# Performance work log

Measured on AMD Instinct MI355X. Metric: run time of the kernel, lower is better.

The kernel has to match this reference:

```python
import jax, jax.numpy as jnp
import numpy as np

NUM_GROUPS = 32
EPS = 1e-5


def group_norm(x, weight, bias):
    # x: (B, C, H, W, D); normalize per (group, spatial) per sample
    b, c, h, w, d = x.shape
    g = NUM_GROUPS
    xg = x.reshape(b, g, c // g, h, w, d)
    mean = xg.mean(axis=(2, 3, 4, 5), keepdims=True)
    var = xg.var(axis=(2, 3, 4, 5), keepdims=True)
    xg = (xg - mean) * jax.lax.rsqrt(var + EPS)
    xn = xg.reshape(b, c, h, w, d)
    return xn * weight[None, :, None, None, None] + bias[None, :, None, None, None]


def setup_inputs() -> dict:
    key = jax.random.key(0)
    ks = jax.random.split(key, 7)
    B, C, H, W, D = 4, 128, 16, 16, 16
    x = jax.random.normal(ks[0], (B, C, H, W, D), dtype=jnp.float32)
    gn_w = jnp.ones((C,), dtype=jnp.float32)
    gn_b = jnp.zeros((C,), dtype=jnp.float32)
    s = 1.0 / np.sqrt(C)
    qkv_w = jax.random.uniform(ks[1], (3 * C, C), minval=-s, maxval=s, dtype=jnp.float32)
    qkv_b = jax.random.uniform(ks[2], (3 * C,), minval=-s, maxval=s, dtype=jnp.float32)
    out_w = jax.random.uniform(ks[3], (C, C), minval=-s, maxval=s, dtype=jnp.float32)
    out_b = jax.random.uniform(ks[4], (C,), minval=-s, maxval=s, dtype=jnp.float32)
    return {"x": x, "gn_w": gn_w, "gn_b": gn_b, "qkv_w": qkv_w,
            "qkv_b": qkv_b, "out_w": out_w, "out_b": out_b}


def reference(x, gn_w, gn_b, qkv_w, qkv_b, out_w, out_b):
    b, c, h, w, d = x.shape
    n = h * w * d
    xn = group_norm(x, gn_w, gn_b)
    # 1x1x1 conv == pointwise linear over channels
    qkv = jnp.einsum('bchwd,oc->bohwd', xn, qkv_w) + qkv_b[None, :, None, None, None]
    q, k, v = jnp.split(qkv, 3, axis=1)
    q = q.transpose(0, 2, 3, 4, 1).reshape(b, n, c)   # (b, n, c)
    k = k.reshape(b, c, n)                             # (b, c, n)
    v = v.transpose(0, 2, 3, 4, 1).reshape(b, n, c)   # (b, n, c)
    scores = jnp.einsum('bnc,bcm->bnm', q, k) * (c ** -0.5)
    attn = jax.nn.softmax(scores, axis=-1)
    out = jnp.einsum('bnm,bmc->bnc', attn, v)          # (b, n, c)
    out = out.reshape(b, h, w, d, c).transpose(0, 4, 1, 2, 3)
    out = jnp.einsum('bchwd,oc->bohwd', out, out_w) + out_b[None, :, None, None, None]
    return out + x
```

## Files before the change

kernel.cpp:

```cpp
#include <hip/hip_runtime.h>

typedef unsigned short u16;
typedef __attribute__((ext_vector_type(8))) short bf16x8;
typedef __attribute__((ext_vector_type(4))) float f32x4;

__device__ __forceinline__ u16 f2bf(float f) {
    union { float f; unsigned u; } v; v.f = f;
    unsigned r = v.u + 0x7fffu + ((v.u >> 16) & 1u);
    return (u16)(r >> 16);
}

__device__ __forceinline__ void gload16(const u16* g, char* l) {
    __builtin_amdgcn_global_load_lds(
        (const __attribute__((address_space(1))) unsigned int*)g,
        (__attribute__((address_space(3))) unsigned int*)l, 16, 0, 0);
}

__global__ __launch_bounds__(256)
void k_stats(const float* __restrict__ x, float* __restrict__ mean, float* __restrict__ rstd)
{
    int bg = blockIdx.x, t = threadIdx.x;
    const float4* xp = (const float4*)(x + (size_t)bg * 16384);
    float s1 = 0.f, s2 = 0.f;
#pragma unroll
    for (int i = 0; i < 16; ++i) {
        float4 v = xp[i * 256 + t];
        s1 += v.x + v.y + v.z + v.w;
        s2 += v.x * v.x + v.y * v.y + v.z * v.z + v.w * v.w;
    }
#pragma unroll
    for (int off = 32; off >= 1; off >>= 1) {
        s1 += __shfl_xor(s1, off);
        s2 += __shfl_xor(s2, off);
    }
    __shared__ float a1[4], a2[4];
    if ((t & 63) == 0) { a1[t >> 6] = s1; a2[t >> 6] = s2; }
    __syncthreads();
    if (t == 0) {
        float t1 = a1[0] + a1[1] + a1[2] + a1[3];
        float t2 = a2[0] + a2[1] + a2[2] + a2[3];
        float mu = t1 * (1.f / 16384.f);
        float var = t2 * (1.f / 16384.f) - mu * mu;
        mean[bg] = mu;
        rstd[bg] = rsqrtf(var + 1e-5f);
    }
}

__global__ __launch_bounds__(384)
void k_qkv(const float* __restrict__ x, const float* __restrict__ gn_w, const float* __restrict__ gn_b,
           const float* __restrict__ qkv_w, const float* __restrict__ qkv_b,
           const float* __restrict__ mean, const float* __restrict__ rstd,
           u16* __restrict__ Qo, u16* __restrict__ Ko, u16* __restrict__ Vo)
{
    __shared__ float xn[128][64];
    int t = threadIdx.x;
    int b = blockIdx.x >> 6;
    int n0 = (blockIdx.x & 63) << 6;

    for (int e = t; e < 8192; e += 384) {
        int c = e >> 6, nn = e & 63;
        int bg = (b << 5) + (c >> 2);
        float sc = rstd[bg] * gn_w[c];
        float sh = gn_b[c] - mean[bg] * sc;
        xn[c][nn] = x[(size_t)(b * 128 + c) * 4096 + n0 + nn] * sc + sh;
    }
    __syncthreads();

    const int og = t >> 2;
    const int ng = t & 3;

    float acc[4][16];
#pragma unroll
    for (int i = 0; i < 4; ++i) {
        float bs = qkv_b[og * 4 + i];
#pragma unroll
        for (int j = 0; j < 16; ++j) acc[i][j] = bs;
    }

    const float4* wr0 = (const float4*)(qkv_w + (size_t)(og * 4 + 0) * 128);
    const float4* wr1 = (const float4*)(qkv_w + (size_t)(og * 4 + 1) * 128);
    const float4* wr2 = (const float4*)(qkv_w + (size_t)(og * 4 + 2) * 128);
    const float4* wr3 = (const float4*)(qkv_w + (size_t)(og * 4 + 3) * 128);

    for (int c4 = 0; c4 < 32; ++c4) {
        float4 w0 = wr0[c4], w1 = wr1[c4], w2 = wr2[c4], w3 = wr3[c4];
#pragma unroll
        for (int cc = 0; cc < 4; ++cc) {
            int c = c4 * 4 + cc;
            float v0 = (cc == 0) ? w0.x : (cc == 1) ? w0.y : (cc == 2) ? w0.z : w0.w;
            float v1 = (cc == 0) ? w1.x : (cc == 1) ? w1.y : (cc == 2) ? w1.z : w1.w;
            float v2 = (cc == 0) ? w2.x : (cc == 1) ? w2.y : (cc == 2) ? w2.z : w2.w;
            float v3 = (cc == 0) ? w3.x : (cc == 1) ? w3.y : (cc == 2) ? w3.z : w3.w;
#pragma unroll
            for (int j4 = 0; j4 < 4; ++j4) {
                float4 xv = *(const float4*)&xn[c][ng * 16 + j4 * 4];
#pragma unroll
                for (int jj = 0; jj < 4; ++jj) {
                    float xs = (jj == 0) ? xv.x : (jj == 1) ? xv.y : (jj == 2) ? xv.z : xv.w;
                    acc[0][j4 * 4 + jj] = fmaf(xs, v0, acc[0][j4 * 4 + jj]);
                    acc[1][j4 * 4 + jj] = fmaf(xs, v1, acc[1][j4 * 4 + jj]);
                    acc[2][j4 * 4 + jj] = fmaf(xs, v2, acc[2][j4 * 4 + jj]);
                    acc[3][j4 * 4 + jj] = fmaf(xs, v3, acc[3][j4 * 4 + jj]);
                }
            }
        }
    }

    const float qscale = 0.08838834764831845f * 1.4426950408889634f;
    if (og < 32) {
        size_t base = (size_t)(b * 4096 + n0 + ng * 16) * 128 + og * 4;
#pragma unroll
        for (int n = 0; n < 16; ++n) {
            uint2 pk;
            pk.x = ((unsigned)f2bf(acc[1][n] * qscale) << 16) | f2bf(acc[0][n] * qscale);
            pk.y = ((unsigned)f2bf(acc[3][n] * qscale) << 16) | f2bf(acc[2][n] * qscale);
            *(uint2*)&Qo[base + (size_t)n * 128] = pk;
        }
    } else if (og < 64) {
        size_t base = (size_t)(b * 4096 + n0 + ng * 16) * 128 + (og - 32) * 4;
#pragma unroll
        for (int n = 0; n < 16; ++n) {
            uint2 pk;
            pk.x = ((unsigned)f2bf(acc[1][n]) << 16) | f2bf(acc[0][n]);
            pk.y = ((unsigned)f2bf(acc[3][n]) << 16) | f2bf(acc[2][n]);
            *(uint2*)&Ko[base + (size_t)n * 128] = pk;
        }
    } else {
#pragma unroll
        for (int i = 0; i < 4; ++i) {
            size_t base = (size_t)(b * 128 + (og - 64) * 4 + i) * 4096 + n0 + ng * 16;
            uint4 pa, pb;
            pa.x = ((unsigned)f2bf(acc[i][1]) << 16) | f2bf(acc[i][0]);
            pa.y = ((unsigned)f2bf(acc[i][3]) << 16) | f2bf(acc[i][2]);
            pa.z = ((unsigned)f2bf(acc[i][5]) << 16) | f2bf(acc[i][4]);
            pa.w = ((unsigned)f2bf(acc[i][7]) << 16) | f2bf(acc[i][6]);
            pb.x = ((unsigned)f2bf(acc[i][9]) << 16) | f2bf(acc[i][8]);
            pb.y = ((unsigned)f2bf(acc[i][11]) << 16) | f2bf(acc[i][10]);
            pb.z = ((unsigned)f2bf(acc[i][13]) << 16) | f2bf(acc[i][12]);
            pb.w = ((unsigned)f2bf(acc[i][15]) << 16) | f2bf(acc[i][14]);
            *(uint4*)&Vo[base] = pa;
            *(uint4*)&Vo[base + 8] = pb;
        }
    }
}

__global__ __launch_bounds__(256, 2)
void k_attn(const u16* __restrict__ Qg, const u16* __restrict__ Kg, const u16* __restrict__ Vg,
            float* __restrict__ Opart, float* __restrict__ ml,
            int split, int kvlen, int iters)
{
    __shared__ __align__(16) u16 Kl[2][64 * 128];
    __shared__ __align__(16) u16 Vl[2][128 * 64];
    __shared__ __align__(16) u16 Pl[4 * 32 * 64];

    const int t = threadIdx.x;
    const int blk = blockIdx.x;
    const int half = blk % split;
    const int qt = (blk / split) & 31;
    const int b = blk / (split * 32);
    const int w = t >> 6;
    const int lane = t & 63;
    const int l15 = lane & 15;
    const int l4 = lane >> 4;
    const int q0 = qt << 7;
    const int swz = (l15 & 7) << 4;

    bf16x8 qf[2][4];
#pragma unroll
    for (int qh = 0; qh < 2; ++qh) {
        const u16* qb = Qg + (size_t)(b * 4096 + q0 + w * 32 + qh * 16 + l15) * 128 + l4 * 8;
#pragma unroll
        for (int kc = 0; kc < 4; ++kc) qf[qh][kc] = *(const bf16x8*)(qb + kc * 32);
    }
    f32x4 oac[2][8];
#pragma unroll
    for (int qh = 0; qh < 2; ++qh)
#pragma unroll
        for (int cf = 0; cf < 8; ++cf) oac[qh][cf] = (f32x4){0.f, 0.f, 0.f, 0.f};
    float m[2] = {-__builtin_inff(), -__builtin_inff()};
    float lsum[2] = {0.f, 0.f};

    const int kv0 = half * kvlen;
    char* plw = (char*)Pl + w * 4096;

    const int krow = lane >> 4;
    const int vrow = lane >> 3;
    const int kcolA = ((lane & 15) ^ krow) * 8;
    const int kcolB = ((lane & 15) ^ (krow + 4)) * 8;
    const int vcol  = ((lane & 7) ^ (vrow & 7)) * 8;
    const u16* KgB = Kg + (size_t)b * 4096 * 128;
    const u16* VgB = Vg + (size_t)b * 128 * 4096;

    auto STAGE = [&](int buf, int kvb) {
        char* kd = (char*)&Kl[buf][0] + w * 4096;
        char* vd = (char*)&Vl[buf][0] + w * 4096;
        const u16* kga = KgB + (size_t)(kvb + 16 * w) * 128;
        const u16* vga = VgB + kvb + (size_t)(32 * w) * 4096;
#pragma unroll
        for (int i = 0; i < 4; ++i) {
            gload16(kga + (size_t)(4 * i + krow) * 128 + ((i & 1) ? kcolB : kcolA),
                    kd + i * 1024);
            gload16(vga + (size_t)(8 * i + vrow) * 4096 + vcol,
                    vd + i * 1024);
        }
    };

    STAGE(0, kv0);
    __syncthreads();

    int cur = 0;
    for (int it = 0; it < iters; ++it) {
        if (it + 1 < iters) STAGE(cur ^ 1, kv0 + (it + 1) * 64);

        const char* kb = (const char*)&Kl[cur][0];
        f32x4 st[2][4];
        __builtin_amdgcn_s_setprio(1);
#pragma unroll
        for (int mt = 0; mt < 4; ++mt) {
            f32x4 s0 = (f32x4){0.f, 0.f, 0.f, 0.f};
            f32x4 s1 = (f32x4){0.f, 0.f, 0.f, 0.f};
#pragma unroll
            for (int kc = 0; kc < 4; ++kc) {
                bf16x8 kf = *(const bf16x8*)(kb + (mt * 16 + l15) * 256 +
                                             ((kc * 64 + l4 * 16) ^ swz));
                s0 = __builtin_amdgcn_mfma_f32_16x16x32_bf16(kf, qf[0][kc], s0, 0, 0, 0);
                s1 = __builtin_amdgcn_mfma_f32_16x16x32_bf16(kf, qf[1][kc], s1, 0, 0, 0);
            }
            st[0][mt] = s0;
            st[1][mt] = s1;
        }
        __builtin_amdgcn_s_setprio(0);

#pragma unroll
        for (int qh = 0; qh < 2; ++qh) {
            float pmax = -__builtin_inff();
#pragma unroll
            for (int mt = 0; mt < 4; ++mt)
                pmax = fmaxf(pmax, fmaxf(fmaxf(st[qh][mt][0], st[qh][mt][1]),
                                         fmaxf(st[qh][mt][2], st[qh][mt][3])));
            pmax = fmaxf(pmax, __shfl_xor(pmax, 16));
            pmax = fmaxf(pmax, __shfl_xor(pmax, 32));

            if (!__all(pmax - m[qh] <= 8.f)) {
                float nm = fmaxf(m[qh], pmax);
                float fr = __builtin_amdgcn_exp2f(m[qh] - nm);
                m[qh] = nm;
                lsum[qh] *= fr;
#pragma unroll
                for (int cf = 0; cf < 8; ++cf)
#pragma unroll
                    for (int r = 0; r < 4; ++r) oac[qh][cf][r] *= fr;
            }

            float rsum = 0.f;
            uint2 pw[4];
#pragma unroll
            for (int mt = 0; mt < 4; ++mt) {
                float p0 = __builtin_amdgcn_exp2f(st[qh][mt][0] - m[qh]);
                float p1 = __builtin_amdgcn_exp2f(st[qh][mt][1] - m[qh]);
                float p2 = __builtin_amdgcn_exp2f(st[qh][mt][2] - m[qh]);
                float p3 = __builtin_amdgcn_exp2f(st[qh][mt][3] - m[qh]);
                rsum += (p0 + p1) + (p2 + p3);
                pw[mt].x = ((unsigned)f2bf(p1) << 16) | f2bf(p0);
                pw[mt].y = ((unsigned)f2bf(p3) << 16) | f2bf(p2);
            }
            rsum += __shfl_xor(rsum, 16);
            rsum += __shfl_xor(rsum, 32);
            lsum[qh] += rsum;

#pragma unroll
            for (int mt = 0; mt < 4; ++mt)
                *(uint2*)(plw + (qh * 16 + l15) * 128 + ((mt * 32 + l4 * 8) ^ swz)) = pw[mt];
        }
        asm volatile("s_waitcnt lgkmcnt(0)" ::: "memory");
        __builtin_amdgcn_sched_barrier(0);

        const char* vb = (const char*)&Vl[cur][0];
        __builtin_amdgcn_s_setprio(1);
#pragma unroll
        for (int kc2 = 0; kc2 < 2; ++kc2) {
            bf16x8 pf0 = *(const bf16x8*)(plw + (0 * 16 + l15) * 128 + ((kc2 * 64 + l4 * 16) ^ swz));
            bf16x8 pf1 = *(const bf16x8*)(plw + (1 * 16 + l15) * 128 + ((kc2 * 64 + l4 * 16) ^ swz));
#pragma unroll
            for (int cf = 0; cf < 8; ++cf) {
                bf16x8 vf = *(const bf16x8*)(vb + (cf * 16 + l15) * 128 +
                                             ((kc2 * 64 + l4 * 16) ^ swz));
                oac[0][cf] = __builtin_amdgcn_mfma_f32_16x16x32_bf16(vf, pf0, oac[0][cf], 0, 0, 0);
                oac[1][cf] = __builtin_amdgcn_mfma_f32_16x16x32_bf16(vf, pf1, oac[1][cf], 0, 0, 0);
            }
        }
        __builtin_amdgcn_s_setprio(0);
        __syncthreads();
        cur ^= 1;
    }

#pragma unroll
    for (int qh = 0; qh < 2; ++qh) {
        size_t qrow = ((size_t)half * 4 + b) * 4096 + q0 + w * 32 + qh * 16 + l15;
        float* orow = Opart + qrow * 128;
#pragma unroll
        for (int cf = 0; cf < 8; ++cf) {
            float4 v;
            v.x = oac[qh][cf][0]; v.y = oac[qh][cf][1];
            v.z = oac[qh][cf][2]; v.w = oac[qh][cf][3];
            *(float4*)&orow[cf * 16 + l4 * 4] = v;
        }
        if (l4 == 0) {
            size_t mb = (size_t)half * 16384 + b * 4096 + q0 + w * 32 + qh * 16 + l15;
            ml[mb * 2 + 0] = m[qh];
            ml[mb * 2 + 1] = lsum[qh];
        }
    }
}

__global__ __launch_bounds__(256)
void k_proj(const float* __restrict__ Opart, const float* __restrict__ ml,
            const float* __restrict__ x, const float* __restrict__ out_w,
            const float* __restrict__ out_b, float* __restrict__ out, int split)
{
    __shared__ float Ol[128][64];
    int t = threadIdx.x;
    int b = blockIdx.x >> 6;
    int n0 = (blockIdx.x & 63) << 6;

    for (int e = t; e < 2048; e += 256) {
        int nn = e >> 5, c4 = e & 31;
        size_t rg = (size_t)b * 4096 + n0 + nn;
        float msv[4], lsv[4];
#pragma unroll
        for (int s = 0; s < 4; ++s) {
            if (s < split) {
                msv[s] = ml[((size_t)s * 16384 + rg) * 2 + 0];
                lsv[s] = ml[((size_t)s * 16384 + rg) * 2 + 1];
            } else { msv[s] = -__builtin_inff(); lsv[s] = 0.f; }
        }
        float mm = fmaxf(fmaxf(msv[0], msv[1]), fmaxf(msv[2], msv[3]));
        float es[4]; float L = 0.f;
#pragma unroll
        for (int s = 0; s < 4; ++s) {
            es[s] = (s < split) ? __builtin_amdgcn_exp2f(msv[s] - mm) : 0.f;
            L += lsv[s] * es[s];
        }
        float inv = 1.f / L;
        float ox = 0.f, oy = 0.f, oz = 0.f, ow = 0.f;
#pragma unroll
        for (int s = 0; s < 4; ++s) {
            if (s < split) {
                float4 o4 = *(const float4*)&Opart[((size_t)s * 16384 + rg) * 128 + c4 * 4];
                ox = fmaf(o4.x, es[s], ox); oy = fmaf(o4.y, es[s], oy);
                oz = fmaf(o4.z, es[s], oz); ow = fmaf(o4.w, es[s], ow);
            }
        }
        Ol[c4 * 4 + 0][nn] = ox * inv;
        Ol[c4 * 4 + 1][nn] = oy * inv;
        Ol[c4 * 4 + 2][nn] = oz * inv;
        Ol[c4 * 4 + 3][nn] = ow * inv;
    }
    __syncthreads();

    const int ocg = t & 31;
    const int ng = t >> 5;

    float acc[4][8];
#pragma unroll
    for (int i = 0; i < 4; ++i) {
        float bs = out_b[ocg * 4 + i];
#pragma unroll
        for (int j = 0; j < 8; ++j) acc[i][j] = bs;
    }

    const float4* wr0 = (const float4*)(out_w + (size_t)(ocg * 4 + 0) * 128);
    const float4* wr1 = (const float4*)(out_w + (size_t)(ocg * 4 + 1) * 128);
    const float4* wr2 = (const float4*)(out_w + (size_t)(ocg * 4 + 2) * 128);
    const float4* wr3 = (const float4*)(out_w + (size_t)(ocg * 4 + 3) * 128);

    for (int c4 = 0; c4 < 32; ++c4) {
        float4 w0 = wr0[c4], w1 = wr1[c4], w2 = wr2[c4], w3 = wr3[c4];
#pragma unroll
        for (int cc = 0; cc < 4; ++cc) {
            int c = c4 * 4 + cc;
            float v0 = (cc == 0) ? w0.x : (cc == 1) ? w0.y : (cc == 2) ? w0.z : w0.w;
            float v1 = (cc == 0) ? w1.x : (cc == 1) ? w1.y : (cc == 2) ? w1.z : w1.w;
            float v2 = (cc == 0) ? w2.x : (cc == 1) ? w2.y : (cc == 2) ? w2.z : w2.w;
            float v3 = (cc == 0) ? w3.x : (cc == 1) ? w3.y : (cc == 2) ? w3.z : w3.w;
#pragma unroll
            for (int j4 = 0; j4 < 2; ++j4) {
                float4 xv = *(const float4*)&Ol[c][ng * 8 + j4 * 4];
#pragma unroll
                for (int jj = 0; jj < 4; ++jj) {
                    float xs = (jj == 0) ? xv.x : (jj == 1) ? xv.y : (jj == 2) ? xv.z : xv.w;
                    acc[0][j4 * 4 + jj] = fmaf(xs, v0, acc[0][j4 * 4 + jj]);
                    acc[1][j4 * 4 + jj] = fmaf(xs, v1, acc[1][j4 * 4 + jj]);
                    acc[2][j4 * 4 + jj] = fmaf(xs, v2, acc[2][j4 * 4 + jj]);
                    acc[3][j4 * 4 + jj] = fmaf(xs, v3, acc[3][j4 * 4 + jj]);
                }
            }
        }
    }

#pragma unroll
    for (int i = 0; i < 4; ++i) {
        size_t ob = (size_t)(b * 128 + ocg * 4 + i) * 4096 + n0 + ng * 8;
#pragma unroll
        for (int j4 = 0; j4 < 2; ++j4) {
            float4 xr = *(const float4*)&x[ob + j4 * 4];
            float4 ov;
            ov.x = acc[i][j4 * 4 + 0] + xr.x;
            ov.y = acc[i][j4 * 4 + 1] + xr.y;
            ov.z = acc[i][j4 * 4 + 2] + xr.z;
            ov.w = acc[i][j4 * 4 + 3] + xr.w;
            *(float4*)&out[ob + j4 * 4] = ov;
        }
    }
}

extern "C" void kernel_launch(void* const* d_in, const int* in_sizes, int n_in,
                              void* d_out, int out_size, void* d_ws, size_t ws_size,
                              hipStream_t stream)
{
    const float* x     = (const float*)d_in[0];
    const float* gn_w  = (const float*)d_in[1];
    const float* gn_b  = (const float*)d_in[2];
    const float* qkv_w = (const float*)d_in[3];
    const float* qkv_b = (const float*)d_in[4];
    const float* out_w = (const float*)d_in[5];
    const float* out_b = (const float*)d_in[6];
    float* out = (float*)d_out;

    char* ws = (char*)d_ws;
    float* mean  = (float*)ws;
    float* rstd  = (float*)(ws + 512);
    u16*   Q     = (u16*)(ws + 4096);
    u16*   K     = (u16*)(ws + 4198400);
    u16*   V     = (u16*)(ws + 8392704);
    float* mlb   = (float*)(ws + 12587008);
    float* Opart = (float*)(ws + 13111296);

    int split = (ws_size >= (size_t)46700000) ? 4 : 2;
    int kvlen = 4096 / split;
    int iters = kvlen / 64;

    k_stats<<<128, 256, 0, stream>>>(x, mean, rstd);
    k_qkv<<<256, 384, 0, stream>>>(x, gn_w, gn_b, qkv_w, qkv_b, mean, rstd, Q, K, V);
    k_attn<<<128 * split, 256, 0, stream>>>(Q, K, V, Opart, mlb, split, kvlen, iters);
    k_proj<<<256, 256, 0, stream>>>(Opart, mlb, x, out_w, out_b, out, split);
}
```

Before: 126.9 us.

## Halve attention KV tile, raise occupancy and split-KV, store partials in bf16

The attention kernel now stages 32-key tiles instead of 64, roughly halving shared memory per block, and raises the launch bound to 4 blocks per CU. Split-KV goes from 4 to 8 (or 2 to 4), giving more blocks to fill the GPU. Partial outputs are written as bf16 instead of fp32, halving partial-buffer traffic between the attention and projection kernels. In exchange there are more loop iterations with a barrier each, more partials to combine, extra rounding error from the bf16 partials, and a removed explicit lgkmcnt wait that the later barrier or compiler must now cover.

Result: slower. 199.6 us (+57.3%).

```diff
diff --git a/kernel.cpp b/kernel.cpp
--- a/kernel.cpp
+++ b/kernel.cpp
@@ -8,6 +8,9 @@
     union { float f; unsigned u; } v; v.f = f;
     unsigned r = v.u + 0x7fffu + ((v.u >> 16) & 1u);
     return (u16)(r >> 16);
+}
+__device__ __forceinline__ float bf2f(unsigned hi16) {
+    union { unsigned u; float f; } v; v.u = hi16 << 16; return v.f;
 }
 
 __device__ __forceinline__ void gload16(const u16* g, char* l) {
@@ -144,14 +147,14 @@
     }
 }
 
-__global__ __launch_bounds__(256, 2)
+__global__ __launch_bounds__(256, 4)
 void k_attn(const u16* __restrict__ Qg, const u16* __restrict__ Kg, const u16* __restrict__ Vg,
-            float* __restrict__ Opart, float* __restrict__ ml,
+            u16* __restrict__ Opart, float* __restrict__ ml,
             int split, int kvlen, int iters)
 {
-    __shared__ __align__(16) u16 Kl[2][64 * 128];
-    __shared__ __align__(16) u16 Vl[2][128 * 64];
-    __shared__ __align__(16) u16 Pl[4 * 32 * 64];
+    __shared__ __align__(16) u16 Kl[2][32 * 128];
+    __shared__ __align__(16) u16 Vl[2][128 * 32];
+    __shared__ __align__(16) u16 Pl[4 * 32 * 32];
 
     const int t = threadIdx.x;
     const int blk = blockIdx.x;
@@ -163,7 +166,8 @@
     const int l15 = lane & 15;
     const int l4 = lane >> 4;
     const int q0 = qt << 7;
-    const int swz = (l15 & 7) << 4;
+    const int swzK = (l15 & 7) << 4;
+    const int swzVP = ((l15 >> 1) & 3) << 4;
 
     bf16x8 qf[2][4];
 #pragma unroll
@@ -181,28 +185,25 @@
     float lsum[2] = {0.f, 0.f};
 
     const int kv0 = half * kvlen;
-    char* plw = (char*)Pl + w * 4096;
+    char* plw = (char*)Pl + w * 2048;
 
     const int krow = lane >> 4;
-    const int vrow = lane >> 3;
     const int kcolA = ((lane & 15) ^ krow) * 8;
     const int kcolB = ((lane & 15) ^ (krow + 4)) * 8;
-    const int vcol  = ((lane & 7) ^ (vrow & 7)) * 8;
+    const int vrow = lane >> 2;
+    const int vcolu = (((lane & 3) ^ ((lane >> 3) & 3))) * 8;
     const u16* KgB = Kg + (size_t)b * 4096 * 128;
     const u16* VgB = Vg + (size_t)b * 128 * 4096;
 
     auto STAGE = [&](int buf, int kvb) {
-        char* kd = (char*)&Kl[buf][0] + w * 4096;
-        char* vd = (char*)&Vl[buf][0] + w * 4096;
-        const u16* kga = KgB + (size_t)(kvb + 16 * w) * 128;
+        char* kd = (char*)&Kl[buf][0] + w * 2048;
+        char* vd = (char*)&Vl[buf][0] + w * 2048;
+        const u16* kga = KgB + (size_t)(kvb + 8 * w) * 128;
         const u16* vga = VgB + kvb + (size_t)(32 * w) * 4096;
-#pragma unroll
-        for (int i = 0; i < 4; ++i) {
-            gload16(kga + (size_t)(4 * i + krow) * 128 + ((i & 1) ? kcolB : kcolA),
-                    kd + i * 1024);
-            gload16(vga + (size_t)(8 * i + vrow) * 4096 + vcol,
-                    vd + i * 1024);
-        }
+        gload16(kga + (size_t)(krow) * 128 + kcolA, kd);
+        gload16(kga + (size_t)(4 + krow) * 128 + kcolB, kd + 1024);
+        gload16(vga + (size_t)(vrow) * 4096 + vcolu, vd);
+        gload16(vga + (size_t)(16 + vrow) * 4096 + vcolu, vd + 1024);
     };
 
     STAGE(0, kv0);
@@ -210,19 +211,19 @@
 
     int cur = 0;
     for (int it = 0; it < iters; ++it) {
-        if (it + 1 < iters) STAGE(cur ^ 1, kv0 + (it + 1) * 64);
+        if (it + 1 < iters) STAGE(cur ^ 1, kv0 + (it + 1) * 32);
 
         const char* kb = (const char*)&Kl[cur][0];
-        f32x4 st[2][4];
+        f32x4 st[2][2];
         __builtin_amdgcn_s_setprio(1);
 #pragma unroll
-        for (int mt = 0; mt < 4; ++mt) {
+        for (int mt = 0; mt < 2; ++mt) {
             f32x4 s0 = (f32x4){0.f, 0.f, 0.f, 0.f};
             f32x4 s1 = (f32x4){0.f, 0.f, 0.f, 0.f};
 #pragma unroll
             for (int kc = 0; kc < 4; ++kc) {
                 bf16x8 kf = *(const bf16x8*)(kb + (mt * 16 + l15) * 256 +
-                                             ((kc * 64 + l4 * 16) ^ swz));
+                                             ((kc * 64 + l4 * 16) ^ swzK));
                 s0 = __builtin_amdgcn_mfma_f32_16x16x32_bf16(kf, qf[0][kc], s0, 0, 0, 0);
                 s1 = __builtin_amdgcn_mfma_f32_16x16x32_bf16(kf, qf[1][kc], s1, 0, 0, 0);
             }
@@ -233,11 +234,10 @@
 
 #pragma unroll
         for (int qh = 0; qh < 2; ++qh) {
-            float pmax = -__builtin_inff();
-#pragma unroll
-            for (int mt = 0; mt < 4; ++mt)
-                pmax = fmaxf(pmax, fmaxf(fmaxf(st[qh][mt][0], st[qh][mt][1]),
-                                         fmaxf(st[qh][mt][2], st[qh][mt][3])));
+            float pmax = fmaxf(fmaxf(fmaxf(st[qh][0][0], st[qh][0][1]),
+                                     fmaxf(st[qh][0][2], st[qh][0][3])),
+                               fmaxf(fmaxf(st[qh][1][0], st[qh][1][1]),
+                                     fmaxf(st[qh][1][2], st[qh][1][3])));
             pmax = fmaxf(pmax, __shfl_xor(pmax, 16));
             pmax = fmaxf(pmax, __shfl_xor(pmax, 32));
 
@@ -253,9 +253,9 @@
             }
 
             float rsum = 0.f;
-            uint2 pw[4];
-#pragma unroll
-            for (int mt = 0; mt < 4; ++mt) {
+            uint2 pw[2];
+#pragma unroll
+            for (int mt = 0; mt < 2; ++mt) {
                 float p0 = __builtin_amdgcn_exp2f(st[qh][mt][0] - m[qh]);
                 float p1 = __builtin_amdgcn_exp2f(st[qh][mt][1] - m[qh]);
                 float p2 = __builtin_amdgcn_exp2f(st[qh][mt][2] - m[qh]);
@@ -269,25 +269,19 @@
             lsum[qh] += rsum;
 
 #pragma unroll
-            for (int mt = 0; mt < 4; ++mt)
-                *(uint2*)(plw + (qh * 16 + l15) * 128 + ((mt * 32 + l4 * 8) ^ swz)) = pw[mt];
-        }
-        asm volatile("s_waitcnt lgkmcnt(0)" ::: "memory");
-        __builtin_amdgcn_sched_barrier(0);
+            for (int mt = 0; mt < 2; ++mt)
+                *(uint2*)(plw + (qh * 16 + l15) * 64 + ((mt * 32 + l4 * 8) ^ swzVP)) = pw[mt];
+        }
 
         const char* vb = (const char*)&Vl[cur][0];
+        bf16x8 pf0 = *(const bf16x8*)(plw + (0 * 16 + l15) * 64 + ((l4 * 16) ^ swzVP));
+        bf16x8 pf1 = *(const bf16x8*)(plw + (1 * 16 + l15) * 64 + ((l4 * 16) ^ swzVP));
         __builtin_amdgcn_s_setprio(1);
 #pragma unroll
-        for (int kc2 = 0; kc2 < 2; ++kc2) {
-            bf16x8 pf0 = *(const bf16x8*)(plw + (0 * 16 + l15) * 128 + ((kc2 * 64 + l4 * 16) ^ swz));
-            bf16x8 pf1 = *(const bf16x8*)(plw + (1 * 16 + l15) * 128 + ((kc2 * 64 + l4 * 16) ^ swz));
-#pragma unroll
-            for (int cf = 0; cf < 8; ++cf) {
-                bf16x8 vf = *(const bf16x8*)(vb + (cf * 16 + l15) * 128 +
-                                             ((kc2 * 64 + l4 * 16) ^ swz));
-                oac[0][cf] = __builtin_amdgcn_mfma_f32_16x16x32_bf16(vf, pf0, oac[0][cf], 0, 0, 0);
-                oac[1][cf] = __builtin_amdgcn_mfma_f32_16x16x32_bf16(vf, pf1, oac[1][cf], 0, 0, 0);
-            }
+        for (int cf = 0; cf < 8; ++cf) {
+            bf16x8 vf = *(const bf16x8*)(vb + (cf * 16 + l15) * 64 + ((l4 * 16) ^ swzVP));
+            oac[0][cf] = __builtin_amdgcn_mfma_f32_16x16x32_bf16(vf, pf0, oac[0][cf], 0, 0, 0);
+            oac[1][cf] = __builtin_amdgcn_mfma_f32_16x16x32_bf16(vf, pf1, oac[1][cf], 0, 0, 0);
         }
         __builtin_amdgcn_s_setprio(0);
         __syncthreads();
@@ -297,13 +291,13 @@
 #pragma unroll
     for (int qh = 0; qh < 2; ++qh) {
         size_t qrow = ((size_t)half * 4 + b) * 4096 + q0 + w * 32 + qh * 16 + l15;
-        float* orow = Opart + qrow * 128;
+        u16* orow = Opart + qrow * 128;
 #pragma unroll
         for (int cf = 0; cf < 8; ++cf) {
-            float4 v;
-            v.x = oac[qh][cf][0]; v.y = oac[qh][cf][1];
-            v.z = oac[qh][cf][2]; v.w = oac[qh][cf][3];
-            *(float4*)&orow[cf * 16 + l4 * 4] = v;
+            uint2 pk;
+            pk.x = ((unsigned)f2bf(oac[qh][cf][1]) << 16) | f2bf(oac[qh][cf][0]);
+            pk.y = ((unsigned)f2bf(oac[qh][cf][3]) << 16) | f2bf(oac[qh][cf][2]);
+            *(uint2*)&orow[cf * 16 + l4 * 4] = pk;
         }
         if (l4 == 0) {
             size_t mb = (size_t)half * 16384 + b * 4096 + q0 + w * 32 + qh * 16 + l15;
@@ -314,7 +308,7 @@
 }
 
 __global__ __launch_bounds__(256)
-void k_proj(const float* __restrict__ Opart, const float* __restrict__ ml,
+void k_proj(const u16* __restrict__ Opart, const float* __restrict__ ml,
             const float* __restrict__ x, const float* __restrict__ out_w,
             const float* __restrict__ out_b, float* __restrict__ out, int split)
 {
@@ -326,29 +320,32 @@
     for (int e = t; e < 2048; e += 256) {
         int nn = e >> 5, c4 = e & 31;
         size_t rg = (size_t)b * 4096 + n0 + nn;
-        float msv[4], lsv[4];
-#pragma unroll
-        for (int s = 0; s < 4; ++s) {
+        float mm = -__builtin_inff();
+        float msv[8], lsv[8];
+#pragma unroll
+        for (int s = 0; s < 8; ++s) {
             if (s < split) {
                 msv[s] = ml[((size_t)s * 16384 + rg) * 2 + 0];
                 lsv[s] = ml[((size_t)s * 16384 + rg) * 2 + 1];
+                mm = fmaxf(mm, msv[s]);
             } else { msv[s] = -__builtin_inff(); lsv[s] = 0.f; }
         }
-        float mm = fmaxf(fmaxf(msv[0], msv[1]), fmaxf(msv[2], msv[3]));
-        float es[4]; float L = 0.f;
-#pragma unroll
-        for (int s = 0; s < 4; ++s) {
+        float es[8]; float L = 0.f;
+#pragma unroll
+        for (int s = 0; s < 8; ++s) {
             es[s] = (s < split) ? __builtin_amdgcn_exp2f(msv[s] - mm) : 0.f;
             L += lsv[s] * es[s];
         }
         float inv = 1.f / L;
         float ox = 0.f, oy = 0.f, oz = 0.f, ow = 0.f;
 #pragma unroll
-        for (int s = 0; s < 4; ++s) {
+        for (int s = 0; s < 8; ++s) {
             if (s < split) {
-                float4 o4 = *(const float4*)&Opart[((size_t)s * 16384 + rg) * 128 + c4 * 4];
-                ox = fmaf(o4.x, es[s], ox); oy = fmaf(o4.y, es[s], oy);
-                oz = fmaf(o4.z, es[s], oz); ow = fmaf(o4.w, es[s], ow);
+                uint2 o2 = *(const uint2*)&Opart[((size_t)s * 16384 + rg) * 128 + c4 * 4];
+                ox = fmaf(bf2f(o2.x & 0xffffu), es[s], ox);
+                oy = fmaf(bf2f(o2.x >> 16), es[s], oy);
+                oz = fmaf(bf2f(o2.y & 0xffffu), es[s], oz);
+                ow = fmaf(bf2f(o2.y >> 16), es[s], ow);
             }
         }
         Ol[c4 * 4 + 0][nn] = ox * inv;
@@ -434,11 +431,11 @@
     u16*   K     = (u16*)(ws + 4198400);
     u16*   V     = (u16*)(ws + 8392704);
     float* mlb   = (float*)(ws + 12587008);
-    float* Opart = (float*)(ws + 13111296);
-
-    int split = (ws_size >= (size_t)46700000) ? 4 : 2;
+    u16*   Opart = (u16*)(ws + 13635584);
+
+    int split = (ws_size >= (size_t)47190016) ? 8 : 4;
     int kvlen = 4096 / split;
-    int iters = kvlen / 64;
+    int iters = kvlen / 32;
 
     k_stats<<<128, 256, 0, stream>>>(x, mean, rstd);
     k_qkv<<<256, 384, 0, stream>>>(x, gn_w, gn_b, qkv_w, qkv_b, mean, rstd, Q, K, V);
```
